# Kernel tuning notes

Measured on AMD Instinct MI355X. Metric: run time of the kernel, lower is better.

Reference implementation:

```python
import jax, jax.numpy as jnp
from jax import lax
import numpy as np

DN = ('NCH', 'OIH', 'NCH')  # conv dimension numbers


def _dw_conv(x, w, stride, pad):
    # depthwise conv1d: x (B,Cin,T), w (Cout, k), groups = Cin
    C = x.shape[1]
    return lax.conv_general_dilated(x, w[:, None, :], (stride,), [(pad, pad)],
                                    feature_group_count=C, dimension_numbers=DN)


def _polyphase_upsample(x, up_w, ratio=2):
    # faithful to _polyphase_upsample_fused: pad (2,3), grouped conv (C -> C*ratio, k=6),
    # interleave the `ratio` phases along time, crop 2 from each side
    B, C, T = x.shape
    xp = jnp.pad(x, ((0, 0), (0, 0), (2, 3)))
    out = _dw_conv(xp, up_w, 1, 0)                     # (B, C*ratio, T)
    out = out.reshape(B, C, ratio, T).transpose(0, 1, 3, 2).reshape(B, C, ratio * T)
    return out[..., 2:-2]


def _snake_beta(x, alpha, beta):
    # SnakeBeta with alpha_logscale=True: x + (1 - cos(2*e^a*x)) / (2*e^b + 1e-9)
    a = jnp.exp(alpha)[None, :, None]
    inv_2b = 1.0 / (2.0 * jnp.exp(beta)[None, :, None] + 1e-9)
    return x + (1.0 - jnp.cos(2.0 * a * x)) * inv_2b


def _activation1d(x, up_w, down_w, alpha, beta):
    x = _polyphase_upsample(x, up_w, 2)                # (B, C, 2T-4)
    x = _snake_beta(x, alpha, beta)
    return _dw_conv(x, down_w, 2, 5)                   # stride-2 lowpass -> (B, C, T-2)


def _conv1d(x, w, b, dilation, pad):
    y = lax.conv_general_dilated(x, w, (1,), [(pad, pad)], rhs_dilation=(dilation,),
                                 dimension_numbers=DN)
    return y + b[None, :, None]


def setup_inputs() -> dict:
    key = jax.random.key(0)
    ks = jax.random.split(key, 13)
    B, C, T = 8, 512, 8192
    f32 = jnp.float32
    return {
        'x': jax.random.normal(ks[0], (B, C, T), f32),
        'up_w1': jax.random.normal(ks[1], (2 * C, 6), f32) * 0.2,
        'down_w1': jax.random.normal(ks[2], (C, 12), f32) * 0.2,
        'alpha1': jax.random.normal(ks[3], (C,), f32) * 0.1,
        'beta1': jax.random.normal(ks[4], (C,), f32) * 0.1,
        'up_w2': jax.random.normal(ks[5], (2 * C, 6), f32) * 0.2,
        'down_w2': jax.random.normal(ks[6], (C, 12), f32) * 0.2,
        'alpha2': jax.random.normal(ks[7], (C,), f32) * 0.1,
        'beta2': jax.random.normal(ks[8], (C,), f32) * 0.1,
        'c1_w': jax.random.normal(ks[9], (C, C, 3), f32) * 0.01,
        'c1_b': jnp.zeros((C,), f32),
        'c2_w': jax.random.normal(ks[10], (C, C, 3), f32) * 0.01,
        'c2_b': jnp.zeros((C,), f32),
    }


def reference(x, up_w1, down_w1, alpha1, beta1, up_w2, down_w2, alpha2, beta2,
              c1_w, c1_b, c2_w, c2_b):
    # AMPBlock0 forward: a1 -> c1 (dilation=dilation[0]=1, pad=1) -> a2 -> c2 (pad=1) -> residual
    xt = _activation1d(x, up_w1, down_w1, alpha1, beta1)   # (B,C,T-2)
    xt = _conv1d(xt, c1_w, c1_b, 1, 1)                     # (B,C,T-2)
    xt = _activation1d(xt, up_w2, down_w2, alpha2, beta2)  # (B,C,T-4)
    xt = _conv1d(xt, c2_w, c2_b, 1, 1)                     # (B,C,T-4)
    return xt + x[:, :, :xt.shape[2]]
```

## Files before the change

### kernel.cpp

```cpp
#include <hip/hip_runtime.h>
#include <math.h>

#define CC 512
#define BB 8
#define TTOT 8192
#define LEN1 (TTOT - 2)
#define LEN2 (TTOT - 4)
#define GPRE 8
#define GPOST 24
#define PITCH (GPRE + TTOT + GPOST)
#define CHST (PITCH * 32)
#define BST (PITCH * 512)

typedef unsigned short u16;
typedef __bf16 v8bf __attribute__((ext_vector_type(8)));
typedef float v4f __attribute__((ext_vector_type(4)));

__device__ __forceinline__ u16 f2b(float f) {
    unsigned u = __float_as_uint(f);
    unsigned r = (u + 0x7FFFu + ((u >> 16) & 1u)) >> 16;
    return (u16)r;
}
__device__ __forceinline__ float b2f(u16 h) {
    return __uint_as_float(((unsigned)h) << 16);
}
__device__ __forceinline__ void ldsdma16(const void* g, void* l) {
    __builtin_amdgcn_global_load_lds(
        (const __attribute__((address_space(1))) unsigned int*)g,
        (__attribute__((address_space(3))) unsigned int*)l, 16, 0, 0);
}


__global__ __launch_bounds__(256) void wprep_kernel(const float* __restrict__ w,
                                                    u16* __restrict__ wr)
{
    int idx = blockIdx.x * 256 + threadIdx.x;
    int co = idx >> 9, ci = idx & 511;
    const float* s = w + (size_t)idx * 3;
    int g = (ci >> 3) & 3;
    int slot = ((g ^ ((co >> 1) & 3)) << 3) | (ci & 7);
    size_t base = (size_t)(ci >> 5) * 3 * 16384 + (size_t)co * 32 + slot;
#pragma unroll
    for (int k = 0; k < 3; ++k)
        wr[base + (size_t)k * 16384] = f2b(s[k]);
}

__global__ __launch_bounds__(256) void zguard_kernel(u16* x0, int Lstart)
{
    int r = blockIdx.x;
    int b = blockIdx.y;
    int R = (r < GPRE) ? r : (GPRE + Lstart + (r - GPRE));
    unsigned* p = (unsigned*)(x0 + (size_t)b * BST);
    int chunk = threadIdx.x >> 4, off = threadIdx.x & 15;
    p[(size_t)chunk * (CHST / 2) + (size_t)R * 16 + off] = 0u;
}

template<bool TMAJ>
__global__ __launch_bounds__(256) void actS_kernel(
    const void* __restrict__ xin_v,
    u16* __restrict__ yout,
    const float* __restrict__ up_w,
    const float* __restrict__ down_w,
    const float* __restrict__ alpha,
    const float* __restrict__ beta,
    int Lin)
{
    const int Lout = Lin - 2;
    const int smax = 2 * Lin - 4;
    const int tid  = threadIdx.x;
    const int cs   = tid & 31;
    const int tseg = tid >> 5;
    const int chunk = blockIdx.y;
    const int b     = blockIdx.z;
    const int T0    = blockIdx.x * 128;
    const int Tt    = T0 + tseg * 16;
    const int cg    = chunk * 32 + cs;

    __shared__ float xs[32 * 141];

    if (!TMAJ) {
        const float* xcb = (const float*)xin_v + ((size_t)b * CC + chunk * 32) * (size_t)Lin;
        int lane = tid & 63, w = tid >> 6;
#pragma unroll
        for (int rr = 0; rr < 8; ++rr) {
            int c = w * 8 + rr;
            const float* xr = xcb + (size_t)c * Lin;
            for (int i = lane; i < 139; i += 64) {
                int g = T0 - 4 + i;
                xs[c * 141 + i] = (g >= 0 && g < Lin) ? xr[g] : 0.0f;
            }
        }
    } else {
        const u16* xb = (const u16*)xin_v + (size_t)b * BST + (size_t)chunk * CHST;
        int pr = tid & 15, rq = tid >> 4;
#pragma unroll
        for (int r0 = 0; r0 < 139; r0 += 16) {
            int row = r0 + rq;
            if (row < 139) {
                int R = GPRE + T0 - 4 + row;
                unsigned u = *((const unsigned*)(xb + (size_t)R * 32) + pr);
                int p2 = pr * 2;
                int c = (((p2 >> 3) ^ ((R >> 1) & 3)) << 3) | (p2 & 7);
                xs[c * 141 + row]       = b2f((u16)(u & 0xFFFFu));
                xs[(c + 1) * 141 + row] = b2f((u16)(u >> 16));
            }
        }
    }
    __syncthreads();

    const float a     = expf(alpha[cg]);
    const float inv2b = 1.0f / (2.0f * expf(beta[cg]) + 1e-9f);
    float uwa[6], uwb[6], dw[12];
#pragma unroll
    for (int k = 0; k < 6; ++k) {
        uwa[k] = up_w[(2 * cg) * 6 + k];
        uwb[k] = up_w[(2 * cg + 1) * 6 + k];
    }
#pragma unroll
    for (int j = 0; j < 12; ++j) dw[j] = down_w[cg * 12 + j];

    const float* xrow = xs + cs * 141 + tseg * 16;

    float xw[12], sr[12];

    auto sval = [&](int idx) -> float {
        int s  = 2 * Tt - 5 + idx;
        int xo = (idx + 1) >> 1;
        float u = 0.0f;
#pragma unroll
        for (int k = 0; k < 6; ++k) {
            float wk = (idx & 1) ? uwa[k] : uwb[k];
            u = fmaf(xw[(xo + k) % 12], wk, u);
        }
        float v = fmaf(1.0f - __cosf(2.0f * a * u), inv2b, u);
        return (s >= 0 && s < smax) ? v : 0.0f;
    };

#pragma unroll
    for (int j = 0; j < 11; ++j) xw[j] = xrow[j];
    xw[11] = 0.0f;
#pragma unroll
    for (int idx = 0; idx < 10; ++idx) sr[idx] = sval(idx);

    u16* yb = yout + (size_t)b * BST + (size_t)chunk * CHST;

#pragma unroll
    for (int i = 0; i < 16; ++i) {
        xw[(11 + i) % 12] = xrow[11 + i];
        sr[(10 + 2 * i) % 12] = sval(10 + 2 * i);
        sr[(11 + 2 * i) % 12] = sval(11 + 2 * i);
        float y = 0.0f;
#pragma unroll
        for (int j = 0; j < 12; ++j)
            y = fmaf(sr[(2 * i + j) % 12], dw[j], y);
        int t = Tt + i;
        if (t < Lout) {
            int R = GPRE + t;
            int slot = (((cs >> 3) ^ ((R >> 1) & 3)) << 3) | (cs & 7);
            yb[(size_t)R * 32 + slot] = f2b(y);
        }
    }
}

template<int ORIENT>
__global__ __launch_bounds__(256, 3) void convg_kernel(
    const u16* __restrict__ xt,
    const u16* __restrict__ wr,
    const float* __restrict__ bias,
    u16* __restrict__ yt,
    float* __restrict__ out,
    const float* __restrict__ resid,
    int Lout)
{
    const int tid  = threadIdx.x;
    const int lane = tid & 63, wid = tid >> 6;
    const int wt = wid & 1, wc = wid >> 1;
    const int l15 = lane & 15, q = lane >> 4;
    const int t0  = blockIdx.x * 128;
    const int co0 = blockIdx.y * 128;
    const int b   = blockIdx.z;

    __shared__ __align__(16) u16 xsm[136 * 32];
    __shared__ __align__(16) u16 wsm[3 * 128 * 32];

    const u16* xb = xt + (size_t)b * BST;
    const int R0 = GPRE + t0 - 1;

    v4f acc[4][4];
#pragma unroll
    for (int m = 0; m < 4; ++m)
#pragma unroll
        for (int n = 0; n < 4; ++n)
#pragma unroll
            for (int r = 0; r < 4; ++r) acc[m][n][r] = 0.0f;

    for (int cig = 0; cig < 16; ++cig) {
        const u16* xsl = xb + (size_t)cig * CHST + (size_t)R0 * 32;
        const u16* wsl = wr + (size_t)cig * 49152 + (size_t)co0 * 32;

#pragma unroll
        for (int j = 0; j < 3; ++j) {
            int ii = wid + 4 * j;
            if (ii < 9) {
                int task = ii * 64 + lane;
                if (task < 544)
                    ldsdma16(xsl + (size_t)task * 8, xsm + (size_t)ii * 512);
            }
        }
#pragma unroll
        for (int j = 0; j < 6; ++j) {
            int ii = wid + 4 * j;
            ldsdma16(wsl + (size_t)(ii * 64 + lane) * 8 + (size_t)(ii >> 3) * 12288,
                     wsm + (size_t)ii * 512);
        }
        __syncthreads();

#pragma unroll
        for (int k = 0; k < 3; ++k) {
            v8bf wf[4];
#pragma unroll
            for (int n = 0; n < 4; ++n) {
                int co_l = wc * 64 + n * 16 + l15;
                wf[n] = *(const v8bf*)(wsm + ((k * 128 + co_l) << 5)
                                           + ((q ^ ((co_l >> 1) & 3)) << 3));
            }
#pragma unroll
            for (int m = 0; m < 4; ++m) {
                int r = wt * 64 + m * 16 + l15 + k;
                v8bf xf = *(const v8bf*)(xsm + (r << 5)
                                             + ((q ^ (((r + 7) >> 1) & 3)) << 3));
#pragma unroll
                for (int n = 0; n < 4; ++n) {
                    if (ORIENT == 0)
                        acc[m][n] = __builtin_amdgcn_mfma_f32_16x16x32_bf16(
                            xf, wf[n], acc[m][n], 0, 0, 0);
                    else
                        acc[m][n] = __builtin_amdgcn_mfma_f32_16x16x32_bf16(
                            wf[n], xf, acc[m][n], 0, 0, 0);
                }
            }
        }
        __syncthreads();
    }

    if (ORIENT == 0) {
        float bv[4];
#pragma unroll
        for (int n = 0; n < 4; ++n) bv[n] = bias[co0 + wc * 64 + n * 16 + l15];
        u16* yb = yt + (size_t)b * BST;
        int cb = (co0 + wc * 64) >> 5;
#pragma unroll
        for (int m = 0; m < 4; ++m) {
            int tb = t0 + wt * 64 + m * 16;
#pragma unroll
            for (int rg = 0; rg < 4; ++rg) {
                int t = tb + q * 4 + rg;
                if (t < Lout) {
                    int R = GPRE + t;
                    int f = (R >> 1) & 3;
#pragma unroll
                    for (int n = 0; n < 4; ++n) {
                        int cl = ((n & 1) << 4) | l15;
                        int slot = (((cl >> 3) ^ f) << 3) | (cl & 7);
                        yb[(size_t)(cb + (n >> 1)) * CHST + (size_t)R * 32 + slot]
                            = f2b(acc[m][n][rg] + bv[n]);
                    }
                }
            }
        }
    } else {
        float bv[4][4];
#pragma unroll
        for (int n = 0; n < 4; ++n)
#pragma unroll
            for (int rg = 0; rg < 4; ++rg)
                bv[n][rg] = bias[co0 + wc * 64 + n * 16 + q * 4 + rg];
#pragma unroll
        for (int n = 0; n < 4; ++n) {
#pragma unroll
            for (int rg = 0; rg < 4; ++rg) {
                int co = co0 + wc * 64 + n * 16 + q * 4 + rg;
                float* orow = out + ((size_t)b * CC + co) * Lout;
                const float* rrow = resid + ((size_t)b * CC + co) * TTOT;
#pragma unroll
                for (int m = 0; m < 4; ++m) {
                    int t = t0 + wt * 64 + m * 16 + l15;
                    if (t < Lout)
                        orow[t] = acc[m][n][rg] + bv[n][rg] + rrow[t];
                }
            }
        }
    }
}

extern "C" void kernel_launch(void* const* d_in, const int* in_sizes, int n_in,
                              void* d_out, int out_size, void* d_ws, size_t ws_size,
                              hipStream_t stream)
{
    const float* x       = (const float*)d_in[0];
    const float* up_w1   = (const float*)d_in[1];
    const float* down_w1 = (const float*)d_in[2];
    const float* alpha1  = (const float*)d_in[3];
    const float* beta1   = (const float*)d_in[4];
    const float* up_w2   = (const float*)d_in[5];
    const float* down_w2 = (const float*)d_in[6];
    const float* alpha2  = (const float*)d_in[7];
    const float* beta2   = (const float*)d_in[8];
    const float* c1_w    = (const float*)d_in[9];
    const float* c1_b    = (const float*)d_in[10];
    const float* c2_w    = (const float*)d_in[11];
    const float* c2_b    = (const float*)d_in[12];
    float* out = (float*)d_out;

    u16* wr1 = (u16*)d_ws;
    u16* wr2 = wr1 + 786432;
    u16* xTa = wr2 + 786432;
    u16* xTb = xTa + (size_t)BB * BST;

    wprep_kernel<<<1024, 256, 0, stream>>>(c1_w, wr1);
    wprep_kernel<<<1024, 256, 0, stream>>>(c2_w, wr2);
    zguard_kernel<<<dim3(32, 8), 256, 0, stream>>>(xTa, LEN1);
    zguard_kernel<<<dim3(32, 8), 256, 0, stream>>>(xTb, LEN1);

    actS_kernel<false><<<dim3(64, 16, 8), 256, 0, stream>>>(
        (const void*)x, xTa, up_w1, down_w1, alpha1, beta1, TTOT);
    convg_kernel<0><<<dim3(64, 4, 8), 256, 0, stream>>>(
        xTa, wr1, c1_b, xTb, nullptr, nullptr, LEN1);
    zguard_kernel<<<dim3(32, 8), 256, 0, stream>>>(xTa, LEN2);
    actS_kernel<true><<<dim3(64, 16, 8), 256, 0, stream>>>(
        (const void*)xTb, xTa, up_w2, down_w2, alpha2, beta2, LEN1);
    convg_kernel<1><<<dim3(64, 4, 8), 256, 0, stream>>>(
        xTa, wr2, c2_b, nullptr, out, x, LEN2);
}
```

Before: 614.6 us.

## Double actS time tile, vectorize staging loads, split FMA chains

```diff
diff --git a/kernel.cpp b/kernel.cpp
--- a/kernel.cpp
+++ b/kernel.cpp
@@ -56,7 +56,7 @@
 }
 
 template<bool TMAJ>
-__global__ __launch_bounds__(256) void actS_kernel(
+__global__ __launch_bounds__(256, 4) void actS_kernel(
     const void* __restrict__ xin_v,
     u16* __restrict__ yout,
     const float* __restrict__ up_w,
@@ -72,37 +72,58 @@
     const int tseg = tid >> 5;
     const int chunk = blockIdx.y;
     const int b     = blockIdx.z;
-    const int T0    = blockIdx.x * 128;
-    const int Tt    = T0 + tseg * 16;
+    const int T0    = blockIdx.x * 256;
+    const int Tt    = T0 + tseg * 32;
     const int cg    = chunk * 32 + cs;
 
-    __shared__ float xs[32 * 141];
+    __shared__ float xs[32 * 269];
 
     if (!TMAJ) {
         const float* xcb = (const float*)xin_v + ((size_t)b * CC + chunk * 32) * (size_t)Lin;
         int lane = tid & 63, w = tid >> 6;
-#pragma unroll
-        for (int rr = 0; rr < 8; ++rr) {
-            int c = w * 8 + rr;
-            const float* xr = xcb + (size_t)c * Lin;
-            for (int i = lane; i < 139; i += 64) {
-                int g = T0 - 4 + i;
-                xs[c * 141 + i] = (g >= 0 && g < Lin) ? xr[g] : 0.0f;
+        if (T0 >= 4 && T0 + 264 <= Lin) {
+#pragma unroll
+            for (int rr = 0; rr < 8; ++rr) {
+                int c = w * 8 + rr;
+                const float* xr = xcb + (size_t)c * Lin + (T0 - 4);
+                float* xd = xs + c * 269;
+                float2 v0 = ((const float2*)xr)[lane];
+                xd[2 * lane]     = v0.x;
+                xd[2 * lane + 1] = v0.y;
+                float2 v1 = ((const float2*)xr)[64 + lane];
+                xd[128 + 2 * lane] = v1.x;
+                xd[129 + 2 * lane] = v1.y;
+                if (lane < 6) {
+                    float2 v2 = ((const float2*)xr)[128 + lane];
+                    xd[256 + 2 * lane] = v2.x;
+                    xd[257 + 2 * lane] = v2.y;
+                }
+            }
+        } else {
+            for (int rr = 0; rr < 8; ++rr) {
+                int c = w * 8 + rr;
+                const float* xr = xcb + (size_t)c * Lin;
+                for (int i = lane; i < 267; i += 64) {
+                    int g = T0 - 4 + i;
+                    xs[c * 269 + i] = (g >= 0 && g < Lin) ? xr[g] : 0.0f;
+                }
             }
         }
     } else {
         const u16* xb = (const u16*)xin_v + (size_t)b * BST + (size_t)chunk * CHST;
-        int pr = tid & 15, rq = tid >> 4;
-#pragma unroll
-        for (int r0 = 0; r0 < 139; r0 += 16) {
+        int pr = tid & 7, rq = tid >> 3;
+#pragma unroll
+        for (int r0 = 0; r0 < 267; r0 += 32) {
             int row = r0 + rq;
-            if (row < 139) {
+            if (row < 267) {
                 int R = GPRE + T0 - 4 + row;
-                unsigned u = *((const unsigned*)(xb + (size_t)R * 32) + pr);
-                int p2 = pr * 2;
-                int c = (((p2 >> 3) ^ ((R >> 1) & 3)) << 3) | (p2 & 7);
-                xs[c * 141 + row]       = b2f((u16)(u & 0xFFFFu));
-                xs[(c + 1) * 141 + row] = b2f((u16)(u >> 16));
+                ushort4 u4 = *(const ushort4*)(xb + (size_t)R * 32 + pr * 4);
+                int f = (R >> 1) & 3;
+                int cb = (((pr >> 1) ^ f) << 3) | ((pr & 1) << 2);
+                xs[(cb    ) * 269 + row] = b2f(u4.x);
+                xs[(cb + 1) * 269 + row] = b2f(u4.y);
+                xs[(cb + 2) * 269 + row] = b2f(u4.z);
+                xs[(cb + 3) * 269 + row] = b2f(u4.w);
             }
         }
     }
@@ -119,19 +140,20 @@
 #pragma unroll
     for (int j = 0; j < 12; ++j) dw[j] = down_w[cg * 12 + j];
 
-    const float* xrow = xs + cs * 141 + tseg * 16;
+    const float* xrow = xs + cs * 269 + tseg * 32;
 
     float xw[12], sr[12];
 
     auto sval = [&](int idx) -> float {
         int s  = 2 * Tt - 5 + idx;
         int xo = (idx + 1) >> 1;
-        float u = 0.0f;
-#pragma unroll
-        for (int k = 0; k < 6; ++k) {
-            float wk = (idx & 1) ? uwa[k] : uwb[k];
-            u = fmaf(xw[(xo + k) % 12], wk, u);
-        }
+        float ua = xw[(xo + 0) % 12] * ((idx & 1) ? uwa[0] : uwb[0]);
+        ua = fmaf(xw[(xo + 1) % 12], (idx & 1) ? uwa[1] : uwb[1], ua);
+        ua = fmaf(xw[(xo + 2) % 12], (idx & 1) ? uwa[2] : uwb[2], ua);
+        float ub = xw[(xo + 3) % 12] * ((idx & 1) ? uwa[3] : uwb[3]);
+        ub = fmaf(xw[(xo + 4) % 12], (idx & 1) ? uwa[4] : uwb[4], ub);
+        ub = fmaf(xw[(xo + 5) % 12], (idx & 1) ? uwa[5] : uwb[5], ub);
+        float u = ua + ub;
         float v = fmaf(1.0f - __cosf(2.0f * a * u), inv2b, u);
         return (s >= 0 && s < smax) ? v : 0.0f;
     };
@@ -145,14 +167,23 @@
     u16* yb = yout + (size_t)b * BST + (size_t)chunk * CHST;
 
 #pragma unroll
-    for (int i = 0; i < 16; ++i) {
+    for (int i = 0; i < 32; ++i) {
         xw[(11 + i) % 12] = xrow[11 + i];
         sr[(10 + 2 * i) % 12] = sval(10 + 2 * i);
         sr[(11 + 2 * i) % 12] = sval(11 + 2 * i);
-        float y = 0.0f;
-#pragma unroll
-        for (int j = 0; j < 12; ++j)
-            y = fmaf(sr[(2 * i + j) % 12], dw[j], y);
+        float y0 = sr[(2 * i + 0) % 12] * dw[0];
+        y0 = fmaf(sr[(2 * i + 1) % 12], dw[1], y0);
+        y0 = fmaf(sr[(2 * i + 2) % 12], dw[2], y0);
+        float y1 = sr[(2 * i + 3) % 12] * dw[3];
+        y1 = fmaf(sr[(2 * i + 4) % 12], dw[4], y1);
+        y1 = fmaf(sr[(2 * i + 5) % 12], dw[5], y1);
+        float y2 = sr[(2 * i + 6) % 12] * dw[6];
+        y2 = fmaf(sr[(2 * i + 7) % 12], dw[7], y2);
+        y2 = fmaf(sr[(2 * i + 8) % 12], dw[8], y2);
+        float y3 = sr[(2 * i + 9) % 12] * dw[9];
+        y3 = fmaf(sr[(2 * i + 10) % 12], dw[10], y3);
+        y3 = fmaf(sr[(2 * i + 11) % 12], dw[11], y3);
+        float y = (y0 + y1) + (y2 + y3);
         int t = Tt + i;
         if (t < Lout) {
             int R = GPRE + t;
@@ -322,12 +353,12 @@
     zguard_kernel<<<dim3(32, 8), 256, 0, stream>>>(xTa, LEN1);
     zguard_kernel<<<dim3(32, 8), 256, 0, stream>>>(xTb, LEN1);
 
-    actS_kernel<false><<<dim3(64, 16, 8), 256, 0, stream>>>(
+    actS_kernel<false><<<dim3(32, 16, 8), 256, 0, stream>>>(
         (const void*)x, xTa, up_w1, down_w1, alpha1, beta1, TTOT);
     convg_kernel<0><<<dim3(64, 4, 8), 256, 0, stream>>>(
         xTa, wr1, c1_b, xTb, nullptr, nullptr, LEN1);
     zguard_kernel<<<dim3(32, 8), 256, 0, stream>>>(xTa, LEN2);
-    actS_kernel<true><<<dim3(64, 16, 8), 256, 0, stream>>>(
+    actS_kernel<true><<<dim3(32, 16, 8), 256, 0, stream>>>(
         (const void*)xTb, xTa, up_w2, down_w2, alpha2, beta2, LEN1);
     convg_kernel<1><<<dim3(64, 4, 8), 256, 0, stream>>>(
         xTa, wr2, c2_b, nullptr, out, x, LEN2);
```

Measured after the change: 665.9 us. +8.4%, slower.
